# Kernel tuning notes

Hardware: AMD Instinct MI355X
Metric: run time of the kernel (lower is better)

Reference implementation:

```python
import jax, jax.numpy as jnp
import numpy as np
from jax import lax

N, T, D, H = 32, 1024, 512, 512


def setup_inputs() -> dict:
    key = jax.random.key(0)
    k1, k2, k3, k4 = jax.random.split(key, 4)
    x = jax.random.normal(k1, (N, T, D), dtype=jnp.float32)
    h0 = jax.random.normal(k2, (N, H), dtype=jnp.float32)
    Wx = jax.random.normal(k3, (D, 4 * H), dtype=jnp.float32) / np.sqrt(D)
    Wh = jax.random.normal(k4, (H, 4 * H), dtype=jnp.float32) / np.sqrt(H)
    b = jnp.zeros((4 * H,), dtype=jnp.float32)
    return {"x": x, "h0": h0, "Wx": Wx, "Wh": Wh, "b": b}


def reference(x, h0, Wx, Wh, b):
    # Precompute input-to-hidden projection for all timesteps (batched GEMM).
    # Mathematically identical to per-step x_t @ Wx in the original.
    xW = jnp.einsum('ntd,dk->ntk', x, Wx) + b  # (N, T, 4H)
    xW = jnp.swapaxes(xW, 0, 1)                # (T, N, 4H) for scan
    c0 = jnp.zeros_like(h0)

    def step(carry, xw_t):
        h, c = carry
        a = xw_t + h @ Wh                      # (N, 4H)
        a_i, a_f, a_o, a_g = jnp.split(a, 4, axis=1)
        i = jax.nn.sigmoid(a_i)
        f = jax.nn.sigmoid(a_f)
        o = jax.nn.sigmoid(a_o)
        g = jnp.tanh(a_g)
        c_next = f * c + i * g
        h_next = o * jnp.tanh(c_next)
        return (h_next, c_next), h_next

    _, hs = lax.scan(step, (h0, c0), xW)       # hs: (T, N, H)
    return jnp.swapaxes(hs, 0, 1)              # (N, T, H)
```

## Files before the change

kernel.cpp:

```cpp
#include <hip/hip_runtime.h>
#include <cstdint>

typedef _Float16 f16;
typedef f16      f16x8 __attribute__((ext_vector_type(8)));
typedef float    f32x4 __attribute__((ext_vector_type(4)));
typedef uint32_t u32;
typedef u32      u32x4 __attribute__((ext_vector_type(4)));

#define NB    32
#define TT    1024
#define DD    512
#define HH    512
#define NBHH  (NB*HH)
#define NWG   64

__device__ __forceinline__ float fsig(float x) {
    return __builtin_amdgcn_rcpf(1.0f + __expf(-x));
}
__device__ __forceinline__ float ftanh(float x) {
    return 1.0f - 2.0f * __builtin_amdgcn_rcpf(__expf(2.0f * x) + 1.0f);
}


__global__ void k_cast_x(const float* __restrict__ x, f16* __restrict__ x16) {
    int i = (blockIdx.x * 256 + threadIdx.x) * 8;
    float4 a = *(const float4*)(x + i);
    float4 c = *(const float4*)(x + i + 4);
    f16x8 v;
    v[0] = (f16)a.x; v[1] = (f16)a.y; v[2] = (f16)a.z; v[3] = (f16)a.w;
    v[4] = (f16)c.x; v[5] = (f16)c.y; v[6] = (f16)c.z; v[7] = (f16)c.w;
    *(f16x8*)(x16 + i) = v;
}

__global__ void k_perm_w(const float* __restrict__ W, f16* __restrict__ Wp) {
    int tid = blockIdx.x * 256 + threadIdx.x;
    int colp = tid >> 9, k = tid & 511;
    int wg = colp >> 5, c = colp & 31;
    int gate = c & 3, j = c >> 2;
    int col = gate * 512 + wg * 8 + j;
    Wp[tid] = (f16)W[k * 2048 + col];
}

__global__ void k_h0(const float* __restrict__ h0, f16* __restrict__ hb) {
    int i = blockIdx.x * 256 + threadIdx.x;
    hb[i] = (f16)h0[i];
}


__global__ void __launch_bounds__(256, 1) k_lstm(
    const f16* __restrict__ x16, const f16* __restrict__ Wxp,
    const f16* __restrict__ Whp, const float* __restrict__ bb,
    f16* hbuf, u32* flags, float* __restrict__ out)
{
    __shared__ unsigned char lds_h[32768];
    __shared__ u32           lds_pub[256];
    __shared__ float         lds_out[8192];

    const int wg  = blockIdx.x;
    const int tid = threadIdx.x;
    const int w   = tid >> 6;
    const int l   = tid & 63;
    const int mt  = w >> 1, nt = w & 1;
    const int lq  = l >> 4, lc = l & 15;

    const int colp = wg * 32 + nt * 16 + lc;
    const int gate = lc & 3, j_in = lc >> 2;
    const int hcol = wg * 8 + nt * 4 + j_in;
    const int hc8  = nt * 4 + j_in;
    const float bv = bb[gate * 512 + hcol];

    const int arow   = mt * 16 + lc;
    const int rm     = l & 3;
    const int n_mine = mt * 16 + lq * 4 + rm;

    f16x8 Bh[16], Bx[16];
    {
        const f16* ph = Whp + (size_t)colp * 512 + lq * 8;
        const f16* px = Wxp + (size_t)colp * 512 + lq * 8;
        #pragma unroll
        for (int ks = 0; ks < 16; ++ks) {
            Bh[ks] = *(const f16x8*)(ph + ks * 32);
            Bx[ks] = *(const f16x8*)(px + ks * 32);
        }
    }

    const f16* xptr = x16 + (size_t)arow * (TT * DD) + lq * 8;

    float c_reg[4] = {0.f, 0.f, 0.f, 0.f};

    for (int t = 0; t < TT; ++t) {
        f32x4 acc = {bv, bv, bv, bv};
        {
            const f16* xp = xptr + (size_t)t * DD;
            #pragma unroll
            for (int ks = 0; ks < 16; ++ks) {
                f16x8 ax = *(const f16x8*)(xp + ks * 32);
                acc = __builtin_amdgcn_mfma_f32_16x16x32_f16(ax, Bx[ks], acc, 0, 0, 0);
            }
        }
        if (t) {
            const u32* fl = flags + l;
            int guard = 0;
            for (;;) {
                u32 f;
                asm volatile("global_load_dword %0, %1, off sc0 sc1"
                             : "=v"(f) : "v"(fl));
                asm volatile("s_waitcnt vmcnt(0)" ::: "memory");
                if (__all(f >= (u32)t) || ++guard > (1 << 20)) break;
            }
        }
        __builtin_amdgcn_sched_barrier(0);
        {
            const char* gp = (const char*)(hbuf + ((t & 1) ? 0 : NBHH)) + tid * 16;
            u32x4 hv4[8];
            #pragma unroll
            for (int r = 0; r < 8; ++r) {
                const char* p = gp + r * 4096;
                asm volatile("global_load_dwordx4 %0, %1, off sc0 sc1"
                             : "=v"(hv4[r]) : "v"(p));
            }
            asm volatile("s_waitcnt vmcnt(0)" ::: "memory");
            __builtin_amdgcn_sched_barrier(0);
            const int inrow = (tid & 63) * 16;
            #pragma unroll
            for (int r = 0; r < 8; ++r) {
                int row = (tid >> 6) + 4 * r;
                int off = row * 1024 + (inrow ^ ((row & 7) << 4));
                *(u32x4*)&lds_h[off] = hv4[r];
            }
        }
        __syncthreads();
        {
            const int swz   = (arow & 7) << 4;
            const int baseA = arow * 1024;
            #pragma unroll
            for (int ks = 0; ks < 16; ++ks) {
                int inrowA = lq * 16 + ks * 64;
                u32x4 a = *(const u32x4*)&lds_h[baseA + (inrowA ^ swz)];
                acc = __builtin_amdgcn_mfma_f32_16x16x32_f16(
                          __builtin_bit_cast(f16x8, a), Bh[ks], acc, 0, 0, 0);
            }
        }
        float hv = 0.f;
        #pragma unroll
        for (int r = 0; r < 4; ++r) {
            float av = acc[r];
            int base = l & ~3;
            float ai = __shfl(av, base | 0, 64);
            float af = __shfl(av, base | 1, 64);
            float ao = __shfl(av, base | 2, 64);
            float ag = __shfl(av, base | 3, 64);
            float ig = fsig(ai), fg = fsig(af), og = fsig(ao), gg = ftanh(ag);
            float cn = fg * c_reg[r] + ig * gg;
            c_reg[r] = cn;
            float h = og * ftanh(cn);
            if (r == rm) hv = h;
        }
        {
            f16 h16 = (f16)hv;
            lds_pub[n_mine * 8 + hc8] = (u32)__builtin_bit_cast(unsigned short, h16);
            lds_out[(t & 31) * 256 + n_mine * 8 + hc8] = hv;
        }
        __syncthreads();
        if (w == 0) {
            if (tid < 32) {
                const u32* pp = lds_pub + tid * 8;
                u32 p0 = (pp[0] & 0xffffu) | (pp[1] << 16);
                u32 p1 = (pp[2] & 0xffffu) | (pp[3] << 16);
                u32 p2 = (pp[4] & 0xffffu) | (pp[5] << 16);
                u32 p3 = (pp[6] & 0xffffu) | (pp[7] << 16);
                u32x4 pv = {p0, p1, p2, p3};
                f16* hdst = hbuf + ((t & 1) ? NBHH : 0) + tid * HH + wg * 8;
                asm volatile("global_store_dwordx4 %0, %1, off sc0 sc1"
                             :: "v"(hdst), "v"(pv) : "memory");
            }
            asm volatile("s_waitcnt vmcnt(0)" ::: "memory");
            if (tid == 0) {
                u32 fv = (u32)(t + 1);
                u32* mf = flags + wg;
                asm volatile("global_store_dword %0, %1, off sc0 sc1"
                             :: "v"(mf), "v"(fv) : "memory");
            }
        }
        if ((t & 31) == 31) {
            #pragma unroll
            for (int r2 = 0; r2 < 8; ++r2) {
                int tau = tid + 256 * r2;
                int s   = tau >> 6;
                int n2  = (tau >> 1) & 31;
                int hc4 = tau & 1;
                float4 v = *(const float4*)&lds_out[s * 256 + n2 * 8 + hc4 * 4];
                float* op = out + (size_t)n2 * (TT * HH)
                                + (size_t)(t - 31 + s) * HH + wg * 8 + hc4 * 4;
                *(float4*)op = v;
            }
        }
    }
}


extern "C" void kernel_launch(void* const* d_in, const int* in_sizes, int n_in,
                              void* d_out, int out_size, void* d_ws, size_t ws_size,
                              hipStream_t stream)
{
    (void)in_sizes; (void)n_in; (void)out_size; (void)ws_size;
    const float* x  = (const float*)d_in[0];
    const float* h0 = (const float*)d_in[1];
    const float* Wx = (const float*)d_in[2];
    const float* Wh = (const float*)d_in[3];
    const float* b  = (const float*)d_in[4];
    float* out = (float*)d_out;

    char* ws = (char*)d_ws;
    u32* flags = (u32*)ws;
    f16* x16   = (f16*)(ws + (4 << 10));
    f16* Wxp   = (f16*)(ws + (4 << 10) + (32 << 20));
    f16* Whp   = (f16*)(ws + (4 << 10) + (34 << 20));
    f16* hbuf  = (f16*)(ws + (4 << 10) + (36 << 20));

    hipMemsetAsync(flags, 0, 4096, stream);
    k_cast_x<<<8192, 256, 0, stream>>>(x, x16);
    k_perm_w<<<4096, 256, 0, stream>>>(Wx, Wxp);
    k_perm_w<<<4096, 256, 0, stream>>>(Wh, Whp);
    k_h0<<<64, 256, 0, stream>>>(h0, hbuf + NBHH);
    k_lstm<<<NWG, 256, 0, stream>>>(x16, Wxp, Whp, b, hbuf, flags, out);
}
```

Baseline: 4.534 ms.

## Split batch into independent groups of workgroups to shrink cross-WG sync scope

Repartitions the 64 workgroups into 4 independent batch groups of 16, each owning 8 batch rows and 128 hidden columns, so each workgroup only waits on 16 flags and loads an 8-row h slice per step. Each wave now computes two column tiles, with the batch rows padded to 16 inside a zeroed LDS region. This cuts the per-step global h traffic and the scope of the spin barrier. In exchange, half of the MFMA rows do wasted work and each wave holds twice as many weight registers.

```diff
diff --git a/kernel.cpp b/kernel.cpp
--- a/kernel.cpp
+++ b/kernel.cpp
@@ -11,7 +11,6 @@
 #define TT    1024
 #define DD    512
 #define HH    512
-#define NBHH  (NB*HH)
 #define NWG   64
 
 __device__ __forceinline__ float fsig(float x) {
@@ -34,16 +33,18 @@
 
 __global__ void k_perm_w(const float* __restrict__ W, f16* __restrict__ Wp) {
     int tid = blockIdx.x * 256 + threadIdx.x;
-    int colp = tid >> 9, k = tid & 511;
-    int wg = colp >> 5, c = colp & 31;
-    int gate = c & 3, j = c >> 2;
-    int col = gate * 512 + wg * 8 + j;
+    int P = tid >> 9, k = tid & 511;
+    int lc = P & 15, ct = (P >> 4) & 1, w = (P >> 5) & 3, wgi = P >> 7;
+    int hcol = wgi * 32 + w * 8 + ct * 4 + (lc >> 2);
+    int col  = (lc & 3) * 512 + hcol;
     Wp[tid] = (f16)W[k * 2048 + col];
 }
 
 __global__ void k_h0(const float* __restrict__ h0, f16* __restrict__ hb) {
     int i = blockIdx.x * 256 + threadIdx.x;
-    hb[i] = (f16)h0[i];
+    int n = i >> 9, hc = i & 511;
+    int g = n >> 3, r = n & 7;
+    hb[(size_t)g * 8192 + 4096 + r * 512 + hc] = (f16)h0[i];
 }
 
 
@@ -52,54 +53,65 @@
     const f16* __restrict__ Whp, const float* __restrict__ bb,
     f16* hbuf, u32* flags, float* __restrict__ out)
 {
-    __shared__ unsigned char lds_h[32768];
+    __shared__ unsigned char lds_h[16384];
     __shared__ u32           lds_pub[256];
     __shared__ float         lds_out[8192];
 
     const int wg  = blockIdx.x;
+    const int g   = wg >> 4;
+    const int wgi = wg & 15;
     const int tid = threadIdx.x;
     const int w   = tid >> 6;
     const int l   = tid & 63;
-    const int mt  = w >> 1, nt = w & 1;
     const int lq  = l >> 4, lc = l & 15;
 
-    const int colp = wg * 32 + nt * 16 + lc;
     const int gate = lc & 3, j_in = lc >> 2;
-    const int hcol = wg * 8 + nt * 4 + j_in;
-    const int hc8  = nt * 4 + j_in;
-    const float bv = bb[gate * 512 + hcol];
-
-    const int arow   = mt * 16 + lc;
-    const int rm     = l & 3;
-    const int n_mine = mt * 16 + lq * 4 + rm;
-
-    f16x8 Bh[16], Bx[16];
-    {
-        const f16* ph = Whp + (size_t)colp * 512 + lq * 8;
-        const f16* px = Wxp + (size_t)colp * 512 + lq * 8;
+    const int rm   = l & 3;
+
+    float bv[2];
+    #pragma unroll
+    for (int ct = 0; ct < 2; ++ct)
+        bv[ct] = bb[gate * 512 + wgi * 32 + w * 8 + ct * 4 + j_in];
+
+    f16x8 Bh[2][16], Bx[2][16];
+    #pragma unroll
+    for (int ct = 0; ct < 2; ++ct) {
+        const size_t colp = (size_t)(wgi * 128 + w * 32 + ct * 16 + lc);
+        const f16* ph = Whp + colp * 512 + lq * 8;
+        const f16* px = Wxp + colp * 512 + lq * 8;
         #pragma unroll
         for (int ks = 0; ks < 16; ++ks) {
-            Bh[ks] = *(const f16x8*)(ph + ks * 32);
-            Bx[ks] = *(const f16x8*)(px + ks * 32);
+            Bh[ct][ks] = *(const f16x8*)(ph + ks * 32);
+            Bx[ct][ks] = *(const f16x8*)(px + ks * 32);
         }
     }
 
-    const f16* xptr = x16 + (size_t)arow * (TT * DD) + lq * 8;
-
-    float c_reg[4] = {0.f, 0.f, 0.f, 0.f};
+    const int arowx = g * 8 + (lc & 7);
+    const f16* xptr = x16 + (size_t)arowx * (TT * DD) + lq * 8;
+
+    f16* hgrp = hbuf + (size_t)g * 8192;
+    u32* flgrp = flags + g * 16;
+
+    *(u32x4*)&lds_h[8192 + tid * 32]      = u32x4{0, 0, 0, 0};
+    *(u32x4*)&lds_h[8192 + tid * 32 + 16] = u32x4{0, 0, 0, 0};
+    __syncthreads();
+
+    float c_reg[2][4] = {{0.f,0.f,0.f,0.f},{0.f,0.f,0.f,0.f}};
 
     for (int t = 0; t < TT; ++t) {
-        f32x4 acc = {bv, bv, bv, bv};
+        f32x4 acc0 = {bv[0], bv[0], bv[0], bv[0]};
+        f32x4 acc1 = {bv[1], bv[1], bv[1], bv[1]};
         {
             const f16* xp = xptr + (size_t)t * DD;
             #pragma unroll
             for (int ks = 0; ks < 16; ++ks) {
                 f16x8 ax = *(const f16x8*)(xp + ks * 32);
-                acc = __builtin_amdgcn_mfma_f32_16x16x32_f16(ax, Bx[ks], acc, 0, 0, 0);
+                acc0 = __builtin_amdgcn_mfma_f32_16x16x32_f16(ax, Bx[0][ks], acc0, 0, 0, 0);
+                acc1 = __builtin_amdgcn_mfma_f32_16x16x32_f16(ax, Bx[1][ks], acc1, 0, 0, 0);
             }
         }
         if (t) {
-            const u32* fl = flags + l;
+            const u32* fl = flgrp + (l & 15);
             int guard = 0;
             for (;;) {
                 u32 f;
@@ -111,87 +123,87 @@
         }
         __builtin_amdgcn_sched_barrier(0);
         {
-            const char* gp = (const char*)(hbuf + ((t & 1) ? 0 : NBHH)) + tid * 16;
-            u32x4 hv4[8];
-            #pragma unroll
-            for (int r = 0; r < 8; ++r) {
-                const char* p = gp + r * 4096;
-                asm volatile("global_load_dwordx4 %0, %1, off sc0 sc1"
-                             : "=v"(hv4[r]) : "v"(p));
-            }
+            const char* gp = (const char*)(hgrp + ((t & 1) ? 0 : 4096)) + tid * 32;
+            u32x4 h0v, h1v;
+            asm volatile("global_load_dwordx4 %0, %1, off sc0 sc1" : "=v"(h0v) : "v"(gp));
+            asm volatile("global_load_dwordx4 %0, %1, off offset:16 sc0 sc1" : "=v"(h1v) : "v"(gp));
             asm volatile("s_waitcnt vmcnt(0)" ::: "memory");
             __builtin_amdgcn_sched_barrier(0);
-            const int inrow = (tid & 63) * 16;
-            #pragma unroll
-            for (int r = 0; r < 8; ++r) {
-                int row = (tid >> 6) + 4 * r;
-                int off = row * 1024 + (inrow ^ ((row & 7) << 4));
-                *(u32x4*)&lds_h[off] = hv4[r];
-            }
+            const int row   = tid >> 5;
+            const int inrow = (tid & 31) * 32;
+            const int swz   = (row & 7) << 4;
+            *(u32x4*)&lds_h[row * 1024 + ((inrow)      ^ swz)] = h0v;
+            *(u32x4*)&lds_h[row * 1024 + ((inrow + 16) ^ swz)] = h1v;
         }
         __syncthreads();
         {
-            const int swz   = (arow & 7) << 4;
-            const int baseA = arow * 1024;
+            const int baseA = lc * 1024;
+            const int swz   = (lc & 7) << 4;
             #pragma unroll
             for (int ks = 0; ks < 16; ++ks) {
                 int inrowA = lq * 16 + ks * 64;
                 u32x4 a = *(const u32x4*)&lds_h[baseA + (inrowA ^ swz)];
-                acc = __builtin_amdgcn_mfma_f32_16x16x32_f16(
-                          __builtin_bit_cast(f16x8, a), Bh[ks], acc, 0, 0, 0);
-            }
-        }
-        float hv = 0.f;
+                f16x8 af = __builtin_bit_cast(f16x8, a);
+                acc0 = __builtin_amdgcn_mfma_f32_16x16x32_f16(af, Bh[0][ks], acc0, 0, 0, 0);
+                acc1 = __builtin_amdgcn_mfma_f32_16x16x32_f16(af, Bh[1][ks], acc1, 0, 0, 0);
+            }
+        }
         #pragma unroll
-        for (int r = 0; r < 4; ++r) {
-            float av = acc[r];
-            int base = l & ~3;
-            float ai = __shfl(av, base | 0, 64);
-            float af = __shfl(av, base | 1, 64);
-            float ao = __shfl(av, base | 2, 64);
-            float ag = __shfl(av, base | 3, 64);
-            float ig = fsig(ai), fg = fsig(af), og = fsig(ao), gg = ftanh(ag);
-            float cn = fg * c_reg[r] + ig * gg;
-            c_reg[r] = cn;
-            float h = og * ftanh(cn);
-            if (r == rm) hv = h;
-        }
-        {
-            f16 h16 = (f16)hv;
-            lds_pub[n_mine * 8 + hc8] = (u32)__builtin_bit_cast(unsigned short, h16);
-            lds_out[(t & 31) * 256 + n_mine * 8 + hc8] = hv;
+        for (int ct = 0; ct < 2; ++ct) {
+            f32x4 acc = ct ? acc1 : acc0;
+            float hv = 0.f;
+            #pragma unroll
+            for (int r = 0; r < 4; ++r) {
+                float av = acc[r];
+                int base = l & ~3;
+                float ai = __shfl(av, base | 0, 64);
+                float af_ = __shfl(av, base | 1, 64);
+                float ao = __shfl(av, base | 2, 64);
+                float ag = __shfl(av, base | 3, 64);
+                float ig = fsig(ai), fg = fsig(af_), og = fsig(ao), gg = ftanh(ag);
+                float cn = fg * c_reg[ct][r] + ig * gg;
+                c_reg[ct][r] = cn;
+                float h = og * ftanh(cn);
+                if (r == rm) hv = h;
+            }
+            if (lq < 2) {
+                int row_local = lq * 4 + rm;
+                int hcl = w * 8 + ct * 4 + j_in;
+                f16 h16 = (f16)hv;
+                lds_pub[row_local * 32 + hcl] = (u32)__builtin_bit_cast(unsigned short, h16);
+                lds_out[(t & 31) * 256 + row_local * 32 + hcl] = hv;
+            }
         }
         __syncthreads();
         if (w == 0) {
             if (tid < 32) {
-                const u32* pp = lds_pub + tid * 8;
+                const int row = tid >> 2, quad = tid & 3;
+                const u32* pp = lds_pub + row * 32 + quad * 8;
                 u32 p0 = (pp[0] & 0xffffu) | (pp[1] << 16);
                 u32 p1 = (pp[2] & 0xffffu) | (pp[3] << 16);
                 u32 p2 = (pp[4] & 0xffffu) | (pp[5] << 16);
                 u32 p3 = (pp[6] & 0xffffu) | (pp[7] << 16);
                 u32x4 pv = {p0, p1, p2, p3};
-                f16* hdst = hbuf + ((t & 1) ? NBHH : 0) + tid * HH + wg * 8;
+                f16* hdst = hgrp + ((t & 1) ? 4096 : 0) + row * 512 + wgi * 32 + quad * 8;
                 asm volatile("global_store_dwordx4 %0, %1, off sc0 sc1"
                              :: "v"(hdst), "v"(pv) : "memory");
             }
             asm volatile("s_waitcnt vmcnt(0)" ::: "memory");
             if (tid == 0) {
                 u32 fv = (u32)(t + 1);
-                u32* mf = flags + wg;
+                u32* mf = flgrp + wgi;
                 asm volatile("global_store_dword %0, %1, off sc0 sc1"
                              :: "v"(mf), "v"(fv) : "memory");
             }
         }
         if ((t & 31) == 31) {
             #pragma unroll
-            for (int r2 = 0; r2 < 8; ++r2) {
-                int tau = tid + 256 * r2;
-                int s   = tau >> 6;
-                int n2  = (tau >> 1) & 31;
-                int hc4 = tau & 1;
-                float4 v = *(const float4*)&lds_out[s * 256 + n2 * 8 + hc4 * 4];
-                float* op = out + (size_t)n2 * (TT * HH)
-                                + (size_t)(t - 31 + s) * HH + wg * 8 + hc4 * 4;
+            for (int k2 = 0; k2 < 8; ++k2) {
+                int tau = tid + 256 * k2;
+                int s = tau >> 6, r = (tau >> 3) & 7, q = tau & 7;
+                float4 v = *(const float4*)&lds_out[s * 256 + r * 32 + q * 4];
+                float* op = out + (size_t)(g * 8 + r) * (TT * HH)
+                                + (size_t)(t - 31 + s) * HH + wgi * 32 + q * 4;
                 *(float4*)op = v;
             }
         }
@@ -222,6 +234,6 @@
     k_cast_x<<<8192, 256, 0, stream>>>(x, x16);
     k_perm_w<<<4096, 256, 0, stream>>>(Wx, Wxp);
     k_perm_w<<<4096, 256, 0, stream>>>(Wh, Whp);
-    k_h0<<<64, 256, 0, stream>>>(h0, hbuf + NBHH);
+    k_h0<<<64, 256, 0, stream>>>(h0, hbuf);
     k_lstm<<<NWG, 256, 0, stream>>>(x16, Wxp, Whp, b, hbuf, flags, out);
 }
```

Result: slower. 6.560 ms (+44.7%).

## Replace flag-based step barrier with per-element tagged hidden-state publishing

Applied to the files above, without the earlier changes.

Each hidden value is now published as a 32-bit word holding the f16 value and a timestep tag, stored directly by every thread. Readers poll the whole hidden buffer and check with a packed-min reduction that all tags match, so the separate flag array, the second block barrier and the serialized store-then-flag sequence go away. The LDS staging buffer is double-buffered and the speculative bulk load is issued before the x-projection MFMAs so its latency overlaps compute. In exchange, the exchanged data doubles in size, each retry re-reads the full buffer, and correctness relies on 32-bit stores being observed atomically.

```diff
diff --git a/kernel.cpp b/kernel.cpp
--- a/kernel.cpp
+++ b/kernel.cpp
@@ -19,6 +19,9 @@
 }
 __device__ __forceinline__ float ftanh(float x) {
     return 1.0f - 2.0f * __builtin_amdgcn_rcpf(__expf(2.0f * x) + 1.0f);
+}
+__device__ __forceinline__ u32 pkmin(u32 a, u32 b) {
+    u32 d; asm("v_pk_min_u16 %0, %1, %2" : "=v"(d) : "v"(a), "v"(b)); return d;
 }
 
 
@@ -41,20 +44,47 @@
     Wp[tid] = (f16)W[k * 2048 + col];
 }
 
-__global__ void k_h0(const float* __restrict__ h0, f16* __restrict__ hb) {
+__global__ void k_h0(const float* __restrict__ h0, u32* __restrict__ hb32) {
     int i = blockIdx.x * 256 + threadIdx.x;
-    hb[i] = (f16)h0[i];
+    f16 v = (f16)h0[i];
+    hb32[NBHH + i] = (u32)__builtin_bit_cast(unsigned short, v);
+}
+
+
+#define TLD(I, OFF) asm volatile("global_load_dwordx4 %0, %1, off" OFF " sc0 sc1" \
+                                 : "=v"(raw[I]) : "v"(gp))
+__device__ __forceinline__ void issue_bulk(u32x4* raw, const u32* gp) {
+    TLD(0,  "");             TLD(1,  " offset:16");
+    TLD(2,  " offset:32");   TLD(3,  " offset:48");
+    TLD(4,  " offset:64");   TLD(5,  " offset:80");
+    TLD(6,  " offset:96");   TLD(7,  " offset:112");
+    TLD(8,  " offset:128");  TLD(9,  " offset:144");
+    TLD(10, " offset:160");  TLD(11, " offset:176");
+    TLD(12, " offset:192");  TLD(13, " offset:208");
+    TLD(14, " offset:224");  TLD(15, " offset:240");
+}
+#undef TLD
+
+__device__ __forceinline__ u32 tagmin16(const u32x4* raw) {
+    u32 m[16];
+    #pragma unroll
+    for (int i = 0; i < 16; ++i)
+        m[i] = pkmin(pkmin(raw[i][0], raw[i][1]), pkmin(raw[i][2], raw[i][3]));
+    #pragma unroll
+    for (int s = 8; s >= 1; s >>= 1)
+        #pragma unroll
+        for (int i = 0; i < s; ++i) m[i] = pkmin(m[i], m[i + s]);
+    return m[0] >> 16;
 }
 
 
 __global__ void __launch_bounds__(256, 1) k_lstm(
     const f16* __restrict__ x16, const f16* __restrict__ Wxp,
     const f16* __restrict__ Whp, const float* __restrict__ bb,
-    f16* hbuf, u32* flags, float* __restrict__ out)
+    u32* hbuf32, float* __restrict__ out)
 {
-    __shared__ unsigned char lds_h[32768];
-    __shared__ u32           lds_pub[256];
-    __shared__ float         lds_out[8192];
+    __shared__ __align__(16) unsigned char lds_h[2][32768];
+    __shared__ float lds_out[8192];
 
     const int wg  = blockIdx.x;
     const int tid = threadIdx.x;
@@ -72,6 +102,9 @@
     const int arow   = mt * 16 + lc;
     const int rm     = l & 3;
     const int n_mine = mt * 16 + lq * 4 + rm;
+
+    const int brow  = tid >> 3;
+    const int bpart = tid & 7;
 
     f16x8 Bh[16], Bx[16];
     {
@@ -85,10 +118,15 @@
     }
 
     const f16* xptr = x16 + (size_t)arow * (TT * DD) + lq * 8;
+    u32* pubp = hbuf32 + n_mine * 512 + hcol;
 
     float c_reg[4] = {0.f, 0.f, 0.f, 0.f};
 
     for (int t = 0; t < TT; ++t) {
+        const u32* gp = hbuf32 + (((t & 1) ^ 1) ? NBHH : 0) + brow * 512 + bpart * 64;
+        u32x4 raw[16];
+        issue_bulk(raw, gp);
+
         f32x4 acc = {bv, bv, bv, bv};
         {
             const f16* xp = xptr + (size_t)t * DD;
@@ -98,49 +136,50 @@
                 acc = __builtin_amdgcn_mfma_f32_16x16x32_f16(ax, Bx[ks], acc, 0, 0, 0);
             }
         }
-        if (t) {
-            const u32* fl = flags + l;
+
+        asm volatile("s_waitcnt vmcnt(0)" ::: "memory");
+        __builtin_amdgcn_sched_barrier(0);
+        {
+            const u32 want = (u32)t;
+            u32 tmin = tagmin16(raw);
             int guard = 0;
-            for (;;) {
-                u32 f;
-                asm volatile("global_load_dword %0, %1, off sc0 sc1"
-                             : "=v"(f) : "v"(fl));
+            while (tmin != want && guard < (1 << 20)) {
+                __builtin_amdgcn_s_sleep(1);
+                issue_bulk(raw, gp);
                 asm volatile("s_waitcnt vmcnt(0)" ::: "memory");
-                if (__all(f >= (u32)t) || ++guard > (1 << 20)) break;
+                tmin = tagmin16(raw);
+                ++guard;
             }
         }
         __builtin_amdgcn_sched_barrier(0);
-        {
-            const char* gp = (const char*)(hbuf + ((t & 1) ? 0 : NBHH)) + tid * 16;
-            u32x4 hv4[8];
-            #pragma unroll
-            for (int r = 0; r < 8; ++r) {
-                const char* p = gp + r * 4096;
-                asm volatile("global_load_dwordx4 %0, %1, off sc0 sc1"
-                             : "=v"(hv4[r]) : "v"(p));
-            }
-            asm volatile("s_waitcnt vmcnt(0)" ::: "memory");
-            __builtin_amdgcn_sched_barrier(0);
-            const int inrow = (tid & 63) * 16;
-            #pragma unroll
-            for (int r = 0; r < 8; ++r) {
-                int row = (tid >> 6) + 4 * r;
-                int off = row * 1024 + (inrow ^ ((row & 7) << 4));
-                *(u32x4*)&lds_h[off] = hv4[r];
+
+        {
+            unsigned char* lbase = &lds_h[t & 1][brow * 1024];
+            const int swz = (brow & 7) << 4;
+            #pragma unroll
+            for (int c16 = 0; c16 < 8; ++c16) {
+                u32x4 a = raw[2 * c16], b2 = raw[2 * c16 + 1];
+                u32x4 wv;
+                wv[0] = __builtin_amdgcn_perm(a[1],  a[0],  0x05040100u);
+                wv[1] = __builtin_amdgcn_perm(a[3],  a[2],  0x05040100u);
+                wv[2] = __builtin_amdgcn_perm(b2[1], b2[0], 0x05040100u);
+                wv[3] = __builtin_amdgcn_perm(b2[3], b2[2], 0x05040100u);
+                *(u32x4*)(lbase + ((bpart * 128 + c16 * 16) ^ swz)) = wv;
             }
         }
         __syncthreads();
-        {
-            const int swz   = (arow & 7) << 4;
-            const int baseA = arow * 1024;
+
+        {
+            const unsigned char* abase = &lds_h[t & 1][arow * 1024];
+            const int swzA = (arow & 7) << 4;
             #pragma unroll
             for (int ks = 0; ks < 16; ++ks) {
-                int inrowA = lq * 16 + ks * 64;
-                u32x4 a = *(const u32x4*)&lds_h[baseA + (inrowA ^ swz)];
+                u32x4 a = *(const u32x4*)(abase + ((lq * 16 + ks * 64) ^ swzA));
                 acc = __builtin_amdgcn_mfma_f32_16x16x32_f16(
                           __builtin_bit_cast(f16x8, a), Bh[ks], acc, 0, 0, 0);
             }
         }
+
         float hv = 0.f;
         #pragma unroll
         for (int r = 0; r < 4; ++r) {
@@ -156,36 +195,21 @@
             float h = og * ftanh(cn);
             if (r == rm) hv = h;
         }
+
         {
             f16 h16 = (f16)hv;
-            lds_pub[n_mine * 8 + hc8] = (u32)__builtin_bit_cast(unsigned short, h16);
+            u32 pub = ((u32)(t + 1) << 16) | (u32)__builtin_bit_cast(unsigned short, h16);
+            u32* pdst = pubp + ((t & 1) ? NBHH : 0);
+            asm volatile("global_store_dword %0, %1, off sc0 sc1"
+                         :: "v"(pdst), "v"(pub) : "memory");
             lds_out[(t & 31) * 256 + n_mine * 8 + hc8] = hv;
         }
-        __syncthreads();
-        if (w == 0) {
-            if (tid < 32) {
-                const u32* pp = lds_pub + tid * 8;
-                u32 p0 = (pp[0] & 0xffffu) | (pp[1] << 16);
-                u32 p1 = (pp[2] & 0xffffu) | (pp[3] << 16);
-                u32 p2 = (pp[4] & 0xffffu) | (pp[5] << 16);
-                u32 p3 = (pp[6] & 0xffffu) | (pp[7] << 16);
-                u32x4 pv = {p0, p1, p2, p3};
-                f16* hdst = hbuf + ((t & 1) ? NBHH : 0) + tid * HH + wg * 8;
-                asm volatile("global_store_dwordx4 %0, %1, off sc0 sc1"
-                             :: "v"(hdst), "v"(pv) : "memory");
-            }
-            asm volatile("s_waitcnt vmcnt(0)" ::: "memory");
-            if (tid == 0) {
-                u32 fv = (u32)(t + 1);
-                u32* mf = flags + wg;
-                asm volatile("global_store_dword %0, %1, off sc0 sc1"
-                             :: "v"(mf), "v"(fv) : "memory");
-            }
-        }
+
         if ((t & 31) == 31) {
-            #pragma unroll
-            for (int r2 = 0; r2 < 8; ++r2) {
-                int tau = tid + 256 * r2;
+            __syncthreads();
+            #pragma unroll
+            for (int k2 = 0; k2 < 8; ++k2) {
+                int tau = tid + 256 * k2;
                 int s   = tau >> 6;
                 int n2  = (tau >> 1) & 31;
                 int hc4 = tau & 1;
@@ -212,16 +236,15 @@
     float* out = (float*)d_out;
 
     char* ws = (char*)d_ws;
-    u32* flags = (u32*)ws;
-    f16* x16   = (f16*)(ws + (4 << 10));
-    f16* Wxp   = (f16*)(ws + (4 << 10) + (32 << 20));
-    f16* Whp   = (f16*)(ws + (4 << 10) + (34 << 20));
-    f16* hbuf  = (f16*)(ws + (4 << 10) + (36 << 20));
-
-    hipMemsetAsync(flags, 0, 4096, stream);
+    f16* x16    = (f16*)ws;
+    f16* Wxp    = (f16*)(ws + (32 << 20));
+    f16* Whp    = (f16*)(ws + (34 << 20));
+    u32* hbuf32 = (u32*)(ws + (36 << 20));
+
+    hipMemsetAsync(hbuf32, 0, NBHH * sizeof(u32), stream);
     k_cast_x<<<8192, 256, 0, stream>>>(x, x16);
     k_perm_w<<<4096, 256, 0, stream>>>(Wx, Wxp);
     k_perm_w<<<4096, 256, 0, stream>>>(Wh, Whp);
-    k_h0<<<64, 256, 0, stream>>>(h0, hbuf + NBHH);
-    k_lstm<<<NWG, 256, 0, stream>>>(x16, Wxp, Whp, b, hbuf, flags, out);
-}
+    k_h0<<<64, 256, 0, stream>>>(h0, hbuf32);
+    k_lstm<<<NWG, 256, 0, stream>>>(x16, Wxp, Whp, b, hbuf32, out);
+}
```

Result: slower. 9.594 ms (+111.6%).

## Consolidate LSTM recurrence into 16 larger workgroups with padded flags

Applied to the files above, without the earlier changes.

Changes the persistent recurrent kernel from 64 workgroups of 256 threads to 16 workgroups of 1024 threads, each owning 32 hidden columns instead of 8. This cuts the number of participants in the per-step cross-workgroup flag barrier. Flags are spaced 64 bytes apart and only one wave polls them, with s_sleep between polls. The trade-off is fewer CUs doing the recurrence, more intra-block __syncthreads, and a shorter output staging window of 8 steps.

```diff
diff --git a/kernel.cpp b/kernel.cpp
--- a/kernel.cpp
+++ b/kernel.cpp
@@ -12,7 +12,7 @@
 #define DD    512
 #define HH    512
 #define NBHH  (NB*HH)
-#define NWG   64
+#define NWG   16
 
 __device__ __forceinline__ float fsig(float x) {
     return __builtin_amdgcn_rcpf(1.0f + __expf(-x));
@@ -47,26 +47,27 @@
 }
 
 
-__global__ void __launch_bounds__(256, 1) k_lstm(
+__global__ void __launch_bounds__(1024, 1) k_lstm(
     const f16* __restrict__ x16, const f16* __restrict__ Wxp,
     const f16* __restrict__ Whp, const float* __restrict__ bb,
     f16* hbuf, u32* flags, float* __restrict__ out)
 {
     __shared__ unsigned char lds_h[32768];
-    __shared__ u32           lds_pub[256];
+    __shared__ u32           lds_pub[1024];
     __shared__ float         lds_out[8192];
 
     const int wg  = blockIdx.x;
     const int tid = threadIdx.x;
     const int w   = tid >> 6;
     const int l   = tid & 63;
-    const int mt  = w >> 1, nt = w & 1;
+    const int ct  = w >> 1;
+    const int mt  = w & 1;
     const int lq  = l >> 4, lc = l & 15;
 
-    const int colp = wg * 32 + nt * 16 + lc;
+    const int colp = wg * 128 + ct * 16 + lc;
     const int gate = lc & 3, j_in = lc >> 2;
-    const int hcol = wg * 8 + nt * 4 + j_in;
-    const int hc8  = nt * 4 + j_in;
+    const int hcol = wg * 32 + ct * 4 + j_in;
+    const int hc32 = ct * 4 + j_in;
     const float bv = bb[gate * 512 + hcol];
 
     const int arow   = mt * 16 + lc;
@@ -86,6 +87,9 @@
 
     const f16* xptr = x16 + (size_t)arow * (TT * DD) + lq * 8;
 
+    const int srow  = tid >> 5;
+    const int sbyte = (tid & 31) * 32;
+
     float c_reg[4] = {0.f, 0.f, 0.f, 0.f};
 
     for (int t = 0; t < TT; ++t) {
@@ -99,35 +103,34 @@
             }
         }
         if (t) {
-            const u32* fl = flags + l;
-            int guard = 0;
-            for (;;) {
-                u32 f;
-                asm volatile("global_load_dword %0, %1, off sc0 sc1"
-                             : "=v"(f) : "v"(fl));
-                asm volatile("s_waitcnt vmcnt(0)" ::: "memory");
-                if (__all(f >= (u32)t) || ++guard > (1 << 20)) break;
-            }
+            if (w == 0) {
+                const u32* fl = flags + (l & 15) * 16;
+                int guard = 0;
+                for (;;) {
+                    u32 f;
+                    asm volatile("global_load_dword %0, %1, off sc0 sc1"
+                                 : "=v"(f) : "v"(fl));
+                    asm volatile("s_waitcnt vmcnt(0)" ::: "memory");
+                    if (__all(f >= (u32)t) || ++guard > (1 << 20)) break;
+                    __builtin_amdgcn_s_sleep(1);
+                }
+            }
+            __syncthreads();
         }
         __builtin_amdgcn_sched_barrier(0);
         {
-            const char* gp = (const char*)(hbuf + ((t & 1) ? 0 : NBHH)) + tid * 16;
-            u32x4 hv4[8];
-            #pragma unroll
-            for (int r = 0; r < 8; ++r) {
-                const char* p = gp + r * 4096;
-                asm volatile("global_load_dwordx4 %0, %1, off sc0 sc1"
-                             : "=v"(hv4[r]) : "v"(p));
-            }
+            const char* gp = (const char*)(hbuf + ((t & 1) ? 0 : NBHH))
+                           + srow * 1024 + sbyte;
+            u32x4 h0v, h1v;
+            asm volatile("global_load_dwordx4 %0, %1, off sc0 sc1"
+                         : "=v"(h0v) : "v"(gp));
+            asm volatile("global_load_dwordx4 %0, %1, off offset:16 sc0 sc1"
+                         : "=v"(h1v) : "v"(gp));
             asm volatile("s_waitcnt vmcnt(0)" ::: "memory");
             __builtin_amdgcn_sched_barrier(0);
-            const int inrow = (tid & 63) * 16;
-            #pragma unroll
-            for (int r = 0; r < 8; ++r) {
-                int row = (tid >> 6) + 4 * r;
-                int off = row * 1024 + (inrow ^ ((row & 7) << 4));
-                *(u32x4*)&lds_h[off] = hv4[r];
-            }
+            const int swz = (srow & 7) << 4;
+            *(u32x4*)&lds_h[srow * 1024 + ((sbyte)      ^ swz)] = h0v;
+            *(u32x4*)&lds_h[srow * 1024 + ((sbyte + 16) ^ swz)] = h1v;
         }
         __syncthreads();
         {
@@ -158,40 +161,46 @@
         }
         {
             f16 h16 = (f16)hv;
-            lds_pub[n_mine * 8 + hc8] = (u32)__builtin_bit_cast(unsigned short, h16);
-            lds_out[(t & 31) * 256 + n_mine * 8 + hc8] = hv;
+            lds_pub[n_mine * 32 + hc32] = (u32)__builtin_bit_cast(unsigned short, h16);
+            lds_out[(t & 7) * 1024 + n_mine * 32 + hc32] = hv;
         }
         __syncthreads();
         if (w == 0) {
-            if (tid < 32) {
-                const u32* pp = lds_pub + tid * 8;
+            const int r0   = l >> 2;
+            const int part = l & 3;
+            #pragma unroll
+            for (int half = 0; half < 2; ++half) {
+                int row = r0 + half * 16;
+                const u32* pp = lds_pub + row * 32 + part * 8;
                 u32 p0 = (pp[0] & 0xffffu) | (pp[1] << 16);
                 u32 p1 = (pp[2] & 0xffffu) | (pp[3] << 16);
                 u32 p2 = (pp[4] & 0xffffu) | (pp[5] << 16);
                 u32 p3 = (pp[6] & 0xffffu) | (pp[7] << 16);
                 u32x4 pv = {p0, p1, p2, p3};
-                f16* hdst = hbuf + ((t & 1) ? NBHH : 0) + tid * HH + wg * 8;
+                f16* hdst = hbuf + ((t & 1) ? NBHH : 0)
+                          + row * HH + wg * 32 + part * 8;
                 asm volatile("global_store_dwordx4 %0, %1, off sc0 sc1"
                              :: "v"(hdst), "v"(pv) : "memory");
             }
             asm volatile("s_waitcnt vmcnt(0)" ::: "memory");
-            if (tid == 0) {
+            if (l == 0) {
                 u32 fv = (u32)(t + 1);
-                u32* mf = flags + wg;
+                u32* mf = flags + wg * 16;
                 asm volatile("global_store_dword %0, %1, off sc0 sc1"
                              :: "v"(mf), "v"(fv) : "memory");
             }
         }
-        if ((t & 31) == 31) {
-            #pragma unroll
-            for (int r2 = 0; r2 < 8; ++r2) {
-                int tau = tid + 256 * r2;
-                int s   = tau >> 6;
-                int n2  = (tau >> 1) & 31;
-                int hc4 = tau & 1;
-                float4 v = *(const float4*)&lds_out[s * 256 + n2 * 8 + hc4 * 4];
-                float* op = out + (size_t)n2 * (TT * HH)
-                                + (size_t)(t - 31 + s) * HH + wg * 8 + hc4 * 4;
+        if ((t & 7) == 7) {
+            #pragma unroll
+            for (int k2 = 0; k2 < 2; ++k2) {
+                int tau = tid + 1024 * k2;
+                int s   = tau >> 8;
+                int q4  = tau & 255;
+                int row = q4 >> 3;
+                int cq  = q4 & 7;
+                float4 v = *(const float4*)&lds_out[s * 1024 + row * 32 + cq * 4];
+                float* op = out + (size_t)row * (TT * HH)
+                                + (size_t)(t - 7 + s) * HH + wg * 32 + cq * 4;
                 *(float4*)op = v;
             }
         }
@@ -223,5 +232,5 @@
     k_perm_w<<<4096, 256, 0, stream>>>(Wx, Wxp);
     k_perm_w<<<4096, 256, 0, stream>>>(Wh, Whp);
     k_h0<<<64, 256, 0, stream>>>(h0, hbuf + NBHH);
-    k_lstm<<<NWG, 256, 0, stream>>>(x16, Wxp, Whp, b, hbuf, flags, out);
-}
+    k_lstm<<<NWG, 1024, 0, stream>>>(x16, Wxp, Whp, b, hbuf, flags, out);
+}
```

New measurement: 17.40 ms. 3.84x slower.
